# Kernel tuning notes

Hardware: AMD Instinct MI355X
Metric: run time of the kernel (lower is better)

The kernel has to match this reference:

```python
import jax, jax.numpy as jnp
import numpy as np

SEQ, BATCH, HIDDEN = 2048, 2, 2048
NUM_HEADS = 16
HEAD_DIM = HIDDEN // NUM_HEADS  # 128


def setup_inputs() -> dict:
    key = jax.random.key(0)
    k1, k2, k3, k4, k5 = jax.random.split(key, 5)
    scale = 1.0 / np.sqrt(HIDDEN)
    return {
        "hidden_states": jax.random.normal(k1, (SEQ, BATCH, HIDDEN), dtype=jnp.float32),
        "w_qkv": jax.random.normal(k2, (3 * HIDDEN, HIDDEN), dtype=jnp.float32) * scale,
        "b_qkv": jax.random.normal(k3, (3 * HIDDEN,), dtype=jnp.float32) * 0.01,
        "w_dense": jax.random.normal(k4, (HIDDEN, HIDDEN), dtype=jnp.float32) * scale,
        "b_dense": jax.random.normal(k5, (HIDDEN,), dtype=jnp.float32) * 0.01,
    }


def reference(hidden_states, w_qkv, b_qkv, w_dense, b_dense):
    s, b, H = hidden_states.shape
    nh, d = NUM_HEADS, HEAD_DIM
    norm_factor = jnp.asarray(np.sqrt(d), dtype=hidden_states.dtype)

    # QKV projection: [s, b, 3H] -> [s, b, nh, 3d] -> chunk into q, k, v
    mixed = hidden_states @ w_qkv.T + b_qkv
    mixed = mixed.reshape(s, b, nh, 3 * d)
    q, k, v = jnp.split(mixed, 3, axis=-1)  # each [s, b, nh, d]

    # Causal scaled dot-product attention, materializing [b, nh, sq, sk]
    scores = jnp.einsum("sbhd,tbhd->bhst", q, k) / norm_factor
    causal = jnp.tril(jnp.ones((s, s), dtype=bool))  # [sq, sk]
    scores = jnp.where(causal[None, None, :, :], scores, jnp.asarray(-10000.0, scores.dtype))
    probs = jax.nn.softmax(scores, axis=-1)

    # Context: [s, b, nh, d] -> [s, b, H]
    ctx = jnp.einsum("bhst,tbhd->sbhd", probs, v).reshape(s, b, H)

    # Output projection
    return ctx @ w_dense.T + b_dense
```

## Files before the change

### kernel.cpp

```cpp
#include <hip/hip_runtime.h>
#include <stdint.h>
#include <stddef.h>

#define SEQ   2048
#define BATCH 2
#define HID   2048
#define NH    16
#define HD    128
#define MTOT  (SEQ*BATCH)
#define NQKV  (3*HID)
#define KDIM  HID
#define LOG2E 1.4426950408889634f

#define BK64    64
#define NT64    (KDIM/BK64)

typedef short  bf16x8 __attribute__((ext_vector_type(8)));
typedef float  f32x4  __attribute__((ext_vector_type(4)));

__device__ __forceinline__ unsigned short f2bf(float f) {
  union { float f; uint32_t u; } a; a.f = f;
  uint32_t r = a.u + 0x7fffu + ((a.u >> 16) & 1u);
  return (unsigned short)(r >> 16);
}

__device__ __forceinline__ f32x4 mfma16(bf16x8 a, bf16x8 b, f32x4 c) {
  return __builtin_amdgcn_mfma_f32_16x16x32_bf16(a, b, c, 0, 0, 0);
}

__device__ __forceinline__ void gl_lds16(const unsigned short* g, unsigned short* l) {
  __builtin_amdgcn_global_load_lds(
      (const __attribute__((address_space(1))) void*)g,
      (__attribute__((address_space(3))) void*)l, 16, 0, 0);
}

__global__ void cvt3_f32_bf16(const float* __restrict__ a, unsigned short* __restrict__ oa, int na,
                              const float* __restrict__ b, unsigned short* __restrict__ ob, int nb,
                              const float* __restrict__ c, unsigned short* __restrict__ oc, int nc) {
  int i = blockIdx.x * blockDim.x + threadIdx.x;
  int stride = gridDim.x * blockDim.x;
  int ntot = na + nb + nc;
  for (; i < ntot; i += stride) {
    const float* src; unsigned short* dst; int j;
    if (i < na)           { src = a; dst = oa; j = i; }
    else if (i < na + nb) { src = b; dst = ob; j = i - na; }
    else                  { src = c; dst = oc; j = i - na - nb; }
    float4 f = reinterpret_cast<const float4*>(src)[j];
    ushort4 o;
    o.x = f2bf(f.x); o.y = f2bf(f.y); o.z = f2bf(f.z); o.w = f2bf(f.w);
    reinterpret_cast<ushort4*>(dst)[j] = o;
  }
}


#define QBUFS 28672

#define QSTA(R) gl_lds16(Asrc + (size_t)(R) * KDIM + koff, &db[((R) + w * 8) * 64])
#define QSTB(R) gl_lds16(Bsrc + (size_t)(R) * KDIM + koff, &db[16384 + ((R) + w * 8) * 64])

#define RD_A4(R0_,R1_,R2_,R3_, G, SB) do {                                    \
    R0_ = *(const bf16x8*)&(SB)[abase + (2*(G)    ) * 1024 + ga0];            \
    R1_ = *(const bf16x8*)&(SB)[abase + (2*(G)    ) * 1024 + ga1];            \
    R2_ = *(const bf16x8*)&(SB)[abase + (2*(G) + 1) * 1024 + ga0];            \
    R3_ = *(const bf16x8*)&(SB)[abase + (2*(G) + 1) * 1024 + ga1];            \
  } while (0)

#define RD_B6(BQ, SB) do {                                                    \
    BQ[0] = *(const bf16x8*)&(SB)[bbase + 0 * 1024 + ga0];                    \
    BQ[1] = *(const bf16x8*)&(SB)[bbase + 1 * 1024 + ga0];                    \
    BQ[2] = *(const bf16x8*)&(SB)[bbase + 2 * 1024 + ga0];                    \
    BQ[3] = *(const bf16x8*)&(SB)[bbase + 0 * 1024 + ga1];                    \
    BQ[4] = *(const bf16x8*)&(SB)[bbase + 1 * 1024 + ga1];                    \
    BQ[5] = *(const bf16x8*)&(SB)[bbase + 2 * 1024 + ga1];                    \
  } while (0)

#define QPH(G, A0_,A1_,A2_,A3_, RDOP, STOP, VMOP, BQ) do {                    \
    STOP;                                                                     \
    VMOP;                                                                     \
    asm volatile("s_barrier" ::: "memory");                                   \
    RDOP;                                                                     \
    __builtin_amdgcn_sched_barrier(0);                                        \
    __builtin_amdgcn_s_setprio(1);                                            \
    _Pragma("unroll")                                                         \
    for (int n_ = 0; n_ < 3; ++n_) {                                          \
      acc[2*(G)][n_]     = mfma16(A0_, BQ[n_],     acc[2*(G)][n_]);           \
      acc[2*(G)][n_]     = mfma16(A1_, BQ[n_ + 3], acc[2*(G)][n_]);           \
      acc[2*(G) + 1][n_] = mfma16(A2_, BQ[n_],     acc[2*(G) + 1][n_]);       \
      acc[2*(G) + 1][n_] = mfma16(A3_, BQ[n_ + 3], acc[2*(G) + 1][n_]);       \
    }                                                                         \
    __builtin_amdgcn_sched_barrier(0);                                        \
    __builtin_amdgcn_s_setprio(0);                                            \
    asm volatile("s_barrier" ::: "memory");                                   \
  } while (0)

#define VM4  asm volatile("s_waitcnt vmcnt(4)" ::: "memory")
#define VM2  asm volatile("s_waitcnt vmcnt(2)" ::: "memory")
#define VM0  asm volatile("s_waitcnt vmcnt(0)" ::: "memory")

#define QTILE(SB, BQC, ST0, ST1, ST2, ST3, VP1, VP3, RAOP) do {               \
    QPH(0, aX0,aX1,aX2,aX3, RD_A4(aY0,aY1,aY2,aY3, 1, SB), ST0, (void)0, BQC);\
    QPH(1, aY0,aY1,aY2,aY3, RD_A4(aX0,aX1,aX2,aX3, 2, SB), ST1, VP1,     BQC);\
    QPH(2, aX0,aX1,aX2,aX3, RD_A4(aY0,aY1,aY2,aY3, 3, SB), ST2, (void)0, BQC);\
    QPH(3, aY0,aY1,aY2,aY3, RAOP,                          ST3, VP3,     BQC);\
  } while (0)

__global__ __launch_bounds__(512, 2) void qkv_gemm(
    const unsigned short* __restrict__ A,
    const unsigned short* __restrict__ B,
    const float* __restrict__ bias,
    unsigned short* __restrict__ Qo,
    unsigned short* __restrict__ Ko,
    unsigned short* __restrict__ Vt)
{
  __shared__ unsigned short smb[2 * QBUFS];
  const int id  = blockIdx.x;
  const int swz = (id & 7) * 64 + (id >> 3);
  const int m0 = (swz >> 5) * 256, n0 = (swz & 31) * 192;
  const int t = threadIdx.x, l = t & 63, w = t >> 6;
  const int wm = w >> 2, wn = w & 3;
  const int fr = l & 15, fg = l >> 4;
  const int abase = (wm * 128 + fr) * 64;
  const int bbase = 16384 + (wn * 48 + fr) * 64;
  const int ga0 = ((fg     ) ^ (fr & 7)) * 8;
  const int ga1 = ((fg + 4 ) ^ (fr & 7)) * 8;
  const int srcrow = w * 8 + (l >> 3);
  const int sgr    = ((l & 7) ^ (l >> 3)) * 8;
  const unsigned short* Asrc = A + (size_t)(m0 + srcrow) * KDIM + sgr;
  const unsigned short* Bsrc = B + (size_t)(n0 + srcrow) * KDIM + sgr;
  unsigned short* const buf0 = smb;
  unsigned short* const buf1 = smb + QBUFS;

  f32x4 acc[8][3] = {};
  bf16x8 aX0, aX1, aX2, aX3, aY0, aY1, aY2, aY3;
  bf16x8 bqE[6], bqO[6];

  {
    unsigned short* db = buf0;
    size_t koff = 0;
    QSTB(0); QSTB(64); QSTB(128);
    QSTA(0); QSTA(128); QSTA(64); QSTA(192);
  }
  VM2;
  asm volatile("s_barrier" ::: "memory");
  RD_B6(bqE, buf0);
  RD_A4(aX0, aX1, aX2, aX3, 0, buf0);

#pragma unroll 1
  for (int tp = 0; tp < 15; ++tp) {
    {
      unsigned short* db = buf1;
      size_t koff = (size_t)(2 * tp + 1) * BK64;
      QTILE(buf0, bqE,
            QSTB(0); QSTB(64),
            QSTB(128); QSTA(0),
            QSTA(128); QSTA(64),
            QSTA(192),
            VM4, VM2,
            RD_B6(bqO, buf1); RD_A4(aX0,aX1,aX2,aX3, 0, buf1));
    }
    {
      unsigned short* db = buf0;
      size_t koff = (size_t)(2 * tp + 2) * BK64;
      QTILE(buf1, bqO,
            QSTB(0); QSTB(64),
            QSTB(128); QSTA(0),
            QSTA(128); QSTA(64),
            QSTA(192),
            VM4, VM2,
            RD_B6(bqE, buf0); RD_A4(aX0,aX1,aX2,aX3, 0, buf0));
    }
  }
  {
    unsigned short* db = buf1;
    size_t koff = (size_t)31 * BK64;
    QTILE(buf0, bqE,
          QSTB(0); QSTB(64),
          QSTB(128); QSTA(0),
          QSTA(128); QSTA(64),
          QSTA(192),
          VM4, VM2,
          RD_B6(bqO, buf1); RD_A4(aX0,aX1,aX2,aX3, 0, buf1));
  }
  {
    QTILE(buf1, bqO,
          (void)0, (void)0, (void)0, (void)0,
          VM0, (void)0,
          (void)0);
  }

#pragma unroll
  for (int n = 0; n < 3; ++n) {
    int ncol = n0 + wn * 48 + n * 16 + fr;
    float bv = bias[ncol];
    int head = ncol / 384;
    int rem  = ncol - head * 384;
    int wi   = rem >> 7;
    int d    = rem & 127;
#pragma unroll
    for (int m = 0; m < 8; ++m) {
#pragma unroll
      for (int j = 0; j < 4; ++j) {
        int r = m0 + wm * 128 + m * 16 + fg * 4 + j;
        int s = r >> 1, bb = r & 1;
        float val = acc[m][n][j] + bv;
        if (wi == 0) {
          val *= 0.08838834764831845f;
          Qo[(((size_t)(bb * NH + head)) * SEQ + s) * HD + d] = f2bf(val);
        } else if (wi == 1) {
          Ko[(((size_t)(bb * NH + head)) * SEQ + s) * HD + d] = f2bf(val);
        } else {
          Vt[(((size_t)(bb * NH + head)) * HD + d) * SEQ + s] = f2bf(val);
        }
      }
    }
  }
}


#define GEMM_PRE()                                                            \
  const int t = threadIdx.x, l = t & 63, w = t >> 6;                          \
  const int wm = w >> 1, wn = w & 1;                                          \
  const int fr = l & 15, fg = l >> 4;                                         \
  const int fx = fr & 7;                                                      \
  const int srow = l >> 3;                                                    \
  const int sgr  = ((l & 7) ^ srow) * 8;                                      \
  const unsigned short* Aw = A + (size_t)(m0 + w * 32 + srow) * KDIM + sgr;   \
  const unsigned short* Bw = B + (size_t)(n0 + w * 16 + srow) * KDIM + sgr;   \
  unsigned short* smb = &sm[0][0];                                            \
  const int a0 = (wm * 64 + fr) * 64 + ((fg ^ fx) * 8);                       \
  const int a1 = (wm * 64 + fr) * 64 + (((4 + fg) ^ fx) * 8);                 \
  const int b0 = 16384 + (wn * 64 + fr) * 64 + ((fg ^ fx) * 8);               \
  const int b1 = 16384 + (wn * 64 + fr) * 64 + (((4 + fg) ^ fx) * 8);         \
  f32x4 acc[4][4] = {};

#define STAGE_AB(KT) do {                                                     \
    unsigned short* dst = &smb[((KT) % 3) * 24576];                           \
    const unsigned short* ap = Aw + (size_t)(KT) * BK64;                      \
    gl_lds16(ap,                    &dst[(w * 4 + 0) * 512]);                 \
    gl_lds16(ap + 8  * KDIM,        &dst[(w * 4 + 1) * 512]);                 \
    gl_lds16(ap + 16 * KDIM,        &dst[(w * 4 + 2) * 512]);                 \
    gl_lds16(ap + 24 * KDIM,        &dst[(w * 4 + 3) * 512]);                 \
    const unsigned short* bp = Bw + (size_t)(KT) * BK64;                      \
    gl_lds16(bp,                    &dst[16384 + (w * 2 + 0) * 512]);         \
    gl_lds16(bp + 8 * KDIM,         &dst[16384 + (w * 2 + 1) * 512]);         \
  } while (0)

#define GEMM_BODY(KT, VM, DOSTAGE) do {                                       \
    const unsigned short* sb = &smb[((KT) % 3) * 24576];                      \
    if (DOSTAGE) STAGE_AB((KT) + 2);                                          \
    bf16x8 af0[4], af1[4], bg0[4], bg1[4];                                    \
    _Pragma("unroll")                                                         \
    for (int m_ = 0; m_ < 4; ++m_) {                                          \
      af0[m_] = *(const bf16x8*)&sb[a0 + m_ * 1024];                          \
      af1[m_] = *(const bf16x8*)&sb[a1 + m_ * 1024];                          \
    }                                                                         \
    _Pragma("unroll")                                                         \
    for (int n_ = 0; n_ < 4; ++n_) {                                          \
      bg0[n_] = *(const bf16x8*)&sb[b0 + n_ * 1024];                          \
      bg1[n_] = *(const bf16x8*)&sb[b1 + n_ * 1024];                          \
    }                                                                         \
    asm volatile("s_waitcnt vmcnt(" #VM ")" ::: "memory");                    \
    asm volatile("s_barrier" ::: "memory");                                   \
    asm volatile("s_waitcnt lgkmcnt(0)" ::: "memory");                        \
    __builtin_amdgcn_sched_barrier(0);                                        \
    __builtin_amdgcn_s_setprio(1);                                            \
    _Pragma("unroll")                                                         \
    for (int m_ = 0; m_ < 4; ++m_)                                            \
      _Pragma("unroll")                                                       \
      for (int n_ = 0; n_ < 4; ++n_)                                          \
        acc[m_][n_] = mfma16(af0[m_], bg0[n_], acc[m_][n_]);                  \
    _Pragma("unroll")                                                         \
    for (int m_ = 0; m_ < 4; ++m_)                                            \
      _Pragma("unroll")                                                       \
      for (int n_ = 0; n_ < 4; ++n_)                                          \
        acc[m_][n_] = mfma16(af1[m_], bg1[n_], acc[m_][n_]);                  \
    __builtin_amdgcn_sched_barrier(0);                                        \
    __builtin_amdgcn_s_setprio(0);                                            \
    asm volatile("s_barrier" ::: "memory");                                   \
  } while (0)

#define GEMM_MAIN()                                                           \
  STAGE_AB(0); STAGE_AB(1);                                                   \
  asm volatile("s_waitcnt vmcnt(6)" ::: "memory");                            \
  asm volatile("s_barrier" ::: "memory");                                     \
  _Pragma("unroll 1")                                                         \
  for (int kt = 0; kt < NT64 - 2; ++kt)                                       \
    GEMM_BODY(kt, 6, 1);                                                      \
  GEMM_BODY(NT64 - 2, 0, 0);                                                  \
  GEMM_BODY(NT64 - 1, 0, 0);

__global__ __launch_bounds__(512, 1) void dense_gemm(
    const unsigned short* __restrict__ A,
    const unsigned short* __restrict__ B,
    const float* __restrict__ bias,
    float* __restrict__ out)
{
  __shared__ unsigned short sm[3][24576];
  int id  = blockIdx.x;
  int swz = (id & 7) * (gridDim.x >> 3) + (id >> 3);
  const int m0 = (swz / 16) * 256, n0 = (swz % 16) * 128;
  GEMM_PRE();
  GEMM_MAIN();

  const int g4 = fg * 4;
#pragma unroll
  for (int n = 0; n < 4; ++n) {
    int ncol = n0 + wn * 64 + n * 16 + fr;
    float bv = bias[ncol];
#pragma unroll
    for (int m = 0; m < 4; ++m) {
#pragma unroll
      for (int j = 0; j < 4; ++j) {
        int r = m0 + wm * 64 + m * 16 + g4 + j;
        out[(size_t)r * HID + ncol] = acc[m][n][j] + bv;
      }
    }
  }
}

__global__ __launch_bounds__(256, 2) void attn_fwd(
    const unsigned short* __restrict__ Q,
    const unsigned short* __restrict__ K,
    const unsigned short* __restrict__ Vt,
    unsigned short* __restrict__ ctx)
{
  __shared__ unsigned short Ksh[2][64 * 128];
  __shared__ unsigned short Vsh[2][128 * 64];
  __shared__ unsigned short Psh[4][16 * 72];
  const int t = threadIdx.x, l = t & 63, w = t >> 6;
  int nwg = gridDim.x * gridDim.y;
  int id  = blockIdx.y * gridDim.x + blockIdx.x;
  int swz = (id & 7) * (nwg >> 3) + (id >> 3);
  const int pair = swz & 15;
  const int bh   = swz >> 4;
  const int qtA = pair, qtB = 31 - pair;
  const int fr = l & 15, fg = l >> 4;
  const size_t base  = (size_t)bh * SEQ * HD;
  const size_t vbase = (size_t)bh * HD * SEQ;

#define STAGE(BUF, KT) do {                                                   \
    const unsigned short* Kt_ = K + base + (size_t)((KT) * 64) * HD;          \
    _Pragma("unroll")                                                         \
    for (int i_ = 0; i_ < 4; ++i_) {                                          \
      int ch_  = w * 4 + i_;                                                  \
      int row_ = ch_ * 4 + (l >> 4);                                          \
      int c16_ = (l & 15) ^ (row_ & 7);                                       \
      gl_lds16(Kt_ + (size_t)row_ * HD + c16_ * 8, &Ksh[BUF][ch_ * 512]);     \
    }                                                                         \
    const unsigned short* Vg_ = Vt + vbase + (KT) * 64;                       \
    _Pragma("unroll")                                                         \
    for (int i_ = 0; i_ < 4; ++i_) {                                          \
      int ch_  = w * 4 + i_;                                                  \
      int row_ = ch_ * 8 + (l >> 3);                                          \
      int c16_ = (l & 7) ^ (row_ & 7);                                        \
      gl_lds16(Vg_ + (size_t)row_ * SEQ + c16_ * 8, &Vsh[BUF][ch_ * 512]);    \
    }                                                                         \
  } while (0)

#define COMPUTE_TILE(QF, OACC, MROW, LROW, QT) do {                           \
    f32x4 sacc[4] = {};                                                       \
    _Pragma("unroll")                                                         \
    for (int c_ = 0; c_ < 4; ++c_) {                                          \
      _Pragma("unroll")                                                       \
      for (int n_ = 0; n_ < 4; ++n_) {                                        \
        int krow = n_ * 16 + fr;                                              \
        int g_   = (c_ * 4 + fg) ^ (krow & 7);                                \
        bf16x8 kf = *(const bf16x8*)&Ksh[buf][krow * 128 + g_ * 8];           \
        sacc[n_] = mfma16(QF[c_], kf, sacc[n_]);                              \
      }                                                                       \
    }                                                                         \
    if (kt == (QT)) {                                                         \
      _Pragma("unroll")                                                       \
      for (int n_ = 0; n_ < 4; ++n_)                                          \
        _Pragma("unroll")                                                     \
        for (int j_ = 0; j_ < 4; ++j_)                                        \
          if (n_ * 16 + fr > w * 16 + fg * 4 + j_) sacc[n_][j_] = -1e30f;     \
    }                                                                         \
    float tm_[4];                                                             \
    _Pragma("unroll")                                                         \
    for (int j_ = 0; j_ < 4; ++j_) {                                          \
      float v0 = fmaxf(fmaxf(sacc[0][j_], sacc[1][j_]),                       \
                       fmaxf(sacc[2][j_], sacc[3][j_]));                      \
      v0 = fmaxf(v0, __shfl_xor(v0, 1));                                      \
      v0 = fmaxf(v0, __shfl_xor(v0, 2));                                      \
      v0 = fmaxf(v0, __shfl_xor(v0, 4));                                      \
      v0 = fmaxf(v0, __shfl_xor(v0, 8));                                      \
      tm_[j_] = v0;                                                           \
    }                                                                         \
    float sc_[4], ps_[4];                                                     \
    _Pragma("unroll")                                                         \
    for (int j_ = 0; j_ < 4; ++j_) {                                          \
      float mn_ = fmaxf(MROW[j_], tm_[j_]);                                   \
      sc_[j_] = exp2f((MROW[j_] - mn_) * LOG2E);                              \
      MROW[j_] = mn_;                                                         \
      ps_[j_] = 0.f;                                                          \
    }                                                                         \
    _Pragma("unroll")                                                         \
    for (int n_ = 0; n_ < 4; ++n_)                                            \
      _Pragma("unroll")                                                       \
      for (int j_ = 0; j_ < 4; ++j_) {                                        \
        float p_ = exp2f((sacc[n_][j_] - MROW[j_]) * LOG2E);                  \
        sacc[n_][j_] = p_;                                                    \
        ps_[j_] += p_;                                                        \
      }                                                                       \
    _Pragma("unroll")                                                         \
    for (int j_ = 0; j_ < 4; ++j_) {                                          \
      float s_ = ps_[j_];                                                     \
      s_ += __shfl_xor(s_, 1);                                                \
      s_ += __shfl_xor(s_, 2);                                                \
      s_ += __shfl_xor(s_, 4);                                                \
      s_ += __shfl_xor(s_, 8);                                                \
      LROW[j_] = LROW[j_] * sc_[j_] + s_;                                     \
    }                                                                         \
    _Pragma("unroll")                                                         \
    for (int n_ = 0; n_ < 8; ++n_)                                            \
      _Pragma("unroll")                                                       \
      for (int j_ = 0; j_ < 4; ++j_)                                          \
        OACC[n_][j_] *= sc_[j_];                                              \
    _Pragma("unroll")                                                         \
    for (int n_ = 0; n_ < 4; ++n_)                                            \
      _Pragma("unroll")                                                       \
      for (int j_ = 0; j_ < 4; ++j_)                                          \
        Psh[w][(fg * 4 + j_) * 72 + n_ * 16 + fr] = f2bf(sacc[n_][j_]);       \
    _Pragma("unroll")                                                         \
    for (int ks_ = 0; ks_ < 2; ++ks_) {                                       \
      bf16x8 pf = *(const bf16x8*)&Psh[w][fr * 72 + ks_ * 32 + fg * 8];       \
      _Pragma("unroll")                                                       \
      for (int n_ = 0; n_ < 8; ++n_) {                                        \
        int vrow = n_ * 16 + fr;                                              \
        int g_   = (ks_ * 4 + fg) ^ (vrow & 7);                               \
        bf16x8 vf = *(const bf16x8*)&Vsh[buf][vrow * 64 + g_ * 8];            \
        OACC[n_] = mfma16(pf, vf, OACC[n_]);                                  \
      }                                                                       \
    }                                                                         \
  } while (0)

  bf16x8 qfA[4], qfB[4];
  {
    const unsigned short* qpA = Q + base + (size_t)(qtA * 64 + w * 16 + fr) * HD + fg * 8;
    const unsigned short* qpB = Q + base + (size_t)(qtB * 64 + w * 16 + fr) * HD + fg * 8;
#pragma unroll
    for (int c = 0; c < 4; ++c) {
      qfA[c] = *(const bf16x8*)(qpA + c * 32);
      qfB[c] = *(const bf16x8*)(qpB + c * 32);
    }
  }
  f32x4 oaccA[8] = {}, oaccB[8] = {};
  float mA[4] = {-1e30f, -1e30f, -1e30f, -1e30f};
  float mB[4] = {-1e30f, -1e30f, -1e30f, -1e30f};
  float lA[4] = {0.f, 0.f, 0.f, 0.f};
  float lB[4] = {0.f, 0.f, 0.f, 0.f};

  STAGE(0, 0);
  __syncthreads();
  int buf = 0;
  for (int kt = 0; kt <= qtB; ++kt) {
    if (kt < qtB) STAGE(buf ^ 1, kt + 1);
    COMPUTE_TILE(qfB, oaccB, mB, lB, qtB);
    if (kt <= qtA) COMPUTE_TILE(qfA, oaccA, mA, lA, qtA);
    __syncthreads();
    buf ^= 1;
  }

  const int bb = bh >> 4, h = bh & 15;
#define WRITE_CTX(OACC, LROW, QT) do {                                        \
    _Pragma("unroll")                                                         \
    for (int n_ = 0; n_ < 8; ++n_)                                            \
      _Pragma("unroll")                                                       \
      for (int j_ = 0; j_ < 4; ++j_) {                                        \
        int qrow = (QT) * 64 + w * 16 + fg * 4 + j_;                          \
        float val = OACC[n_][j_] / LROW[j_];                                  \
        ctx[((size_t)(qrow * BATCH + bb)) * HID + h * HD + n_ * 16 + fr] =    \
            f2bf(val);                                                        \
      }                                                                       \
  } while (0)
  WRITE_CTX(oaccA, lA, qtA);
  WRITE_CTX(oaccB, lB, qtB);
#undef STAGE
#undef COMPUTE_TILE
#undef WRITE_CTX
}

extern "C" void kernel_launch(void* const* d_in, const int* in_sizes, int n_in,
                              void* d_out, int out_size, void* d_ws, size_t ws_size,
                              hipStream_t stream) {
  const float* hs      = (const float*)d_in[0];
  const float* w_qkv   = (const float*)d_in[1];
  const float* b_qkv   = (const float*)d_in[2];
  const float* w_dense = (const float*)d_in[3];
  const float* b_dense = (const float*)d_in[4];
  float* out = (float*)d_out;

  unsigned short* hsb = (unsigned short*)d_ws;
  unsigned short* wqb = hsb + (size_t)MTOT * HID;
  unsigned short* wdb = wqb + (size_t)NQKV * HID;
  unsigned short* q   = wdb + (size_t)HID * HID;
  unsigned short* k   = q   + (size_t)MTOT * HID;
  unsigned short* vt  = k   + (size_t)MTOT * HID;
  unsigned short* ctx = vt  + (size_t)MTOT * HID;

  cvt3_f32_bf16<<<2048, 256, 0, stream>>>(
      hs, hsb, (MTOT * HID) / 4,
      w_qkv, wqb, (NQKV * HID) / 4,
      w_dense, wdb, (HID * HID) / 4);

  qkv_gemm<<<dim3((MTOT / 256) * (NQKV / 192)), 512, 0, stream>>>(hsb, wqb, b_qkv, q, k, vt);
  attn_fwd<<<dim3(16, 32), 256, 0, stream>>>(q, k, vt, ctx);
  dense_gemm<<<dim3((MTOT / 256) * (HID / 128)), 512, 0, stream>>>(ctx, wdb, b_dense, out);
}
```

Baseline: 279.9 us.

## Simplify QKV and dense GEMM pipelines to single-barrier double-buffered tiles

Both GEMM main loops are restructured. The QKV GEMM drops its four-phase, eight-barrier ping-pong schedule for a simple double-buffered loop with one barrier and full vmcnt/lgkmcnt drains per K-tile. The dense GEMM goes from a three-stage LDS ring to two buffers, staging the next tile while interleaving A-fragment reads with MFMAs. This cuts barrier and sched_barrier overhead and shrinks LDS use for the dense kernel. In exchange it gives up deeper prefetch and priority tuning, so global-load latency may be exposed once per tile.

Measured after the change: 276.6 us. Within noise of the previous version (-1.2%).

```diff
diff --git a/kernel.cpp b/kernel.cpp
--- a/kernel.cpp
+++ b/kernel.cpp
@@ -57,15 +57,17 @@
 
 #define QSTA(R) gl_lds16(Asrc + (size_t)(R) * KDIM + koff, &db[((R) + w * 8) * 64])
 #define QSTB(R) gl_lds16(Bsrc + (size_t)(R) * KDIM + koff, &db[16384 + ((R) + w * 8) * 64])
-
-#define RD_A4(R0_,R1_,R2_,R3_, G, SB) do {                                    \
-    R0_ = *(const bf16x8*)&(SB)[abase + (2*(G)    ) * 1024 + ga0];            \
-    R1_ = *(const bf16x8*)&(SB)[abase + (2*(G)    ) * 1024 + ga1];            \
-    R2_ = *(const bf16x8*)&(SB)[abase + (2*(G) + 1) * 1024 + ga0];            \
-    R3_ = *(const bf16x8*)&(SB)[abase + (2*(G) + 1) * 1024 + ga1];            \
-  } while (0)
-
-#define RD_B6(BQ, SB) do {                                                    \
+#define QSTAGE7 do { QSTB(0); QSTB(64); QSTB(128);                            \
+                     QSTA(0); QSTA(64); QSTA(128); QSTA(192); } while (0)
+
+#define RD_A4v(R, G, SB) do {                                                 \
+    R[0] = *(const bf16x8*)&(SB)[abase + (2*(G)    ) * 1024 + ga0];           \
+    R[1] = *(const bf16x8*)&(SB)[abase + (2*(G)    ) * 1024 + ga1];           \
+    R[2] = *(const bf16x8*)&(SB)[abase + (2*(G) + 1) * 1024 + ga0];           \
+    R[3] = *(const bf16x8*)&(SB)[abase + (2*(G) + 1) * 1024 + ga1];           \
+  } while (0)
+
+#define RD_B6v(BQ, SB) do {                                                   \
     BQ[0] = *(const bf16x8*)&(SB)[bbase + 0 * 1024 + ga0];                    \
     BQ[1] = *(const bf16x8*)&(SB)[bbase + 1 * 1024 + ga0];                    \
     BQ[2] = *(const bf16x8*)&(SB)[bbase + 2 * 1024 + ga0];                    \
@@ -74,34 +76,31 @@
     BQ[5] = *(const bf16x8*)&(SB)[bbase + 2 * 1024 + ga1];                    \
   } while (0)
 
-#define QPH(G, A0_,A1_,A2_,A3_, RDOP, STOP, VMOP, BQ) do {                    \
-    STOP;                                                                     \
-    VMOP;                                                                     \
+#define MFMA_G(G, R, BQ) do {                                                 \
+    _Pragma("unroll")                                                         \
+    for (int n_ = 0; n_ < 3; ++n_) {                                          \
+      acc[2*(G)][n_]     = mfma16(R[0], BQ[n_],     acc[2*(G)][n_]);          \
+      acc[2*(G)][n_]     = mfma16(R[1], BQ[n_ + 3], acc[2*(G)][n_]);          \
+      acc[2*(G) + 1][n_] = mfma16(R[2], BQ[n_],     acc[2*(G) + 1][n_]);      \
+      acc[2*(G) + 1][n_] = mfma16(R[3], BQ[n_ + 3], acc[2*(G) + 1][n_]);      \
+    }                                                                         \
+  } while (0)
+
+#define QTILE_FF(SB, DOSTAGE) do {                                            \
+    bf16x8 bq[6], aP[4], aQ[4];                                               \
+    RD_B6v(bq, SB);                                                           \
+    RD_A4v(aP, 0, SB);                                                        \
+    RD_A4v(aQ, 1, SB);                                                        \
+    if (DOSTAGE) QSTAGE7;                                                     \
+    MFMA_G(0, aP, bq);                                                        \
+    RD_A4v(aP, 2, SB);                                                        \
+    MFMA_G(1, aQ, bq);                                                        \
+    RD_A4v(aQ, 3, SB);                                                        \
+    MFMA_G(2, aP, bq);                                                        \
+    MFMA_G(3, aQ, bq);                                                        \
+    asm volatile("s_waitcnt lgkmcnt(0)" ::: "memory");                        \
+    asm volatile("s_waitcnt vmcnt(0)" ::: "memory");                          \
     asm volatile("s_barrier" ::: "memory");                                   \
-    RDOP;                                                                     \
-    __builtin_amdgcn_sched_barrier(0);                                        \
-    __builtin_amdgcn_s_setprio(1);                                            \
-    _Pragma("unroll")                                                         \
-    for (int n_ = 0; n_ < 3; ++n_) {                                          \
-      acc[2*(G)][n_]     = mfma16(A0_, BQ[n_],     acc[2*(G)][n_]);           \
-      acc[2*(G)][n_]     = mfma16(A1_, BQ[n_ + 3], acc[2*(G)][n_]);           \
-      acc[2*(G) + 1][n_] = mfma16(A2_, BQ[n_],     acc[2*(G) + 1][n_]);       \
-      acc[2*(G) + 1][n_] = mfma16(A3_, BQ[n_ + 3], acc[2*(G) + 1][n_]);       \
-    }                                                                         \
-    __builtin_amdgcn_sched_barrier(0);                                        \
-    __builtin_amdgcn_s_setprio(0);                                            \
-    asm volatile("s_barrier" ::: "memory");                                   \
-  } while (0)
-
-#define VM4  asm volatile("s_waitcnt vmcnt(4)" ::: "memory")
-#define VM2  asm volatile("s_waitcnt vmcnt(2)" ::: "memory")
-#define VM0  asm volatile("s_waitcnt vmcnt(0)" ::: "memory")
-
-#define QTILE(SB, BQC, ST0, ST1, ST2, ST3, VP1, VP3, RAOP) do {               \
-    QPH(0, aX0,aX1,aX2,aX3, RD_A4(aY0,aY1,aY2,aY3, 1, SB), ST0, (void)0, BQC);\
-    QPH(1, aY0,aY1,aY2,aY3, RD_A4(aX0,aX1,aX2,aX3, 2, SB), ST1, VP1,     BQC);\
-    QPH(2, aX0,aX1,aX2,aX3, RD_A4(aY0,aY1,aY2,aY3, 3, SB), ST2, (void)0, BQC);\
-    QPH(3, aY0,aY1,aY2,aY3, RAOP,                          ST3, VP3,     BQC);\
   } while (0)
 
 __global__ __launch_bounds__(512, 2) void qkv_gemm(
@@ -127,65 +126,23 @@
   const int sgr    = ((l & 7) ^ (l >> 3)) * 8;
   const unsigned short* Asrc = A + (size_t)(m0 + srcrow) * KDIM + sgr;
   const unsigned short* Bsrc = B + (size_t)(n0 + srcrow) * KDIM + sgr;
-  unsigned short* const buf0 = smb;
-  unsigned short* const buf1 = smb + QBUFS;
 
   f32x4 acc[8][3] = {};
-  bf16x8 aX0, aX1, aX2, aX3, aY0, aY1, aY2, aY3;
-  bf16x8 bqE[6], bqO[6];
 
   {
-    unsigned short* db = buf0;
+    unsigned short* db = smb;
     size_t koff = 0;
-    QSTB(0); QSTB(64); QSTB(128);
-    QSTA(0); QSTA(128); QSTA(64); QSTA(192);
-  }
-  VM2;
+    QSTAGE7;
+  }
+  asm volatile("s_waitcnt vmcnt(0)" ::: "memory");
   asm volatile("s_barrier" ::: "memory");
-  RD_B6(bqE, buf0);
-  RD_A4(aX0, aX1, aX2, aX3, 0, buf0);
 
 #pragma unroll 1
-  for (int tp = 0; tp < 15; ++tp) {
-    {
-      unsigned short* db = buf1;
-      size_t koff = (size_t)(2 * tp + 1) * BK64;
-      QTILE(buf0, bqE,
-            QSTB(0); QSTB(64),
-            QSTB(128); QSTA(0),
-            QSTA(128); QSTA(64),
-            QSTA(192),
-            VM4, VM2,
-            RD_B6(bqO, buf1); RD_A4(aX0,aX1,aX2,aX3, 0, buf1));
-    }
-    {
-      unsigned short* db = buf0;
-      size_t koff = (size_t)(2 * tp + 2) * BK64;
-      QTILE(buf1, bqO,
-            QSTB(0); QSTB(64),
-            QSTB(128); QSTA(0),
-            QSTA(128); QSTA(64),
-            QSTA(192),
-            VM4, VM2,
-            RD_B6(bqE, buf0); RD_A4(aX0,aX1,aX2,aX3, 0, buf0));
-    }
-  }
-  {
-    unsigned short* db = buf1;
-    size_t koff = (size_t)31 * BK64;
-    QTILE(buf0, bqE,
-          QSTB(0); QSTB(64),
-          QSTB(128); QSTA(0),
-          QSTA(128); QSTA(64),
-          QSTA(192),
-          VM4, VM2,
-          RD_B6(bqO, buf1); RD_A4(aX0,aX1,aX2,aX3, 0, buf1));
-  }
-  {
-    QTILE(buf1, bqO,
-          (void)0, (void)0, (void)0, (void)0,
-          VM0, (void)0,
-          (void)0);
+  for (int kt = 0; kt < NT64; ++kt) {
+    const unsigned short* sb = &smb[(kt & 1) * QBUFS];
+    unsigned short* db = &smb[((kt + 1) & 1) * QBUFS];
+    size_t koff = (size_t)(kt + 1) * BK64;
+    QTILE_FF(sb, (kt < NT64 - 1));
   }
 
 #pragma unroll
@@ -217,77 +174,49 @@
 }
 
 
-#define GEMM_PRE()                                                            \
-  const int t = threadIdx.x, l = t & 63, w = t >> 6;                          \
-  const int wm = w >> 1, wn = w & 1;                                          \
-  const int fr = l & 15, fg = l >> 4;                                         \
-  const int fx = fr & 7;                                                      \
-  const int srow = l >> 3;                                                    \
-  const int sgr  = ((l & 7) ^ srow) * 8;                                      \
-  const unsigned short* Aw = A + (size_t)(m0 + w * 32 + srow) * KDIM + sgr;   \
-  const unsigned short* Bw = B + (size_t)(n0 + w * 16 + srow) * KDIM + sgr;   \
-  unsigned short* smb = &sm[0][0];                                            \
-  const int a0 = (wm * 64 + fr) * 64 + ((fg ^ fx) * 8);                       \
-  const int a1 = (wm * 64 + fr) * 64 + (((4 + fg) ^ fx) * 8);                 \
-  const int b0 = 16384 + (wn * 64 + fr) * 64 + ((fg ^ fx) * 8);               \
-  const int b1 = 16384 + (wn * 64 + fr) * 64 + (((4 + fg) ^ fx) * 8);         \
-  f32x4 acc[4][4] = {};
-
-#define STAGE_AB(KT) do {                                                     \
-    unsigned short* dst = &smb[((KT) % 3) * 24576];                           \
-    const unsigned short* ap = Aw + (size_t)(KT) * BK64;                      \
-    gl_lds16(ap,                    &dst[(w * 4 + 0) * 512]);                 \
-    gl_lds16(ap + 8  * KDIM,        &dst[(w * 4 + 1) * 512]);                 \
-    gl_lds16(ap + 16 * KDIM,        &dst[(w * 4 + 2) * 512]);                 \
-    gl_lds16(ap + 24 * KDIM,        &dst[(w * 4 + 3) * 512]);                 \
-    const unsigned short* bp = Bw + (size_t)(KT) * BK64;                      \
-    gl_lds16(bp,                    &dst[16384 + (w * 2 + 0) * 512]);         \
-    gl_lds16(bp + 8 * KDIM,         &dst[16384 + (w * 2 + 1) * 512]);         \
-  } while (0)
-
-#define GEMM_BODY(KT, VM, DOSTAGE) do {                                       \
-    const unsigned short* sb = &smb[((KT) % 3) * 24576];                      \
-    if (DOSTAGE) STAGE_AB((KT) + 2);                                          \
-    bf16x8 af0[4], af1[4], bg0[4], bg1[4];                                    \
-    _Pragma("unroll")                                                         \
-    for (int m_ = 0; m_ < 4; ++m_) {                                          \
-      af0[m_] = *(const bf16x8*)&sb[a0 + m_ * 1024];                          \
-      af1[m_] = *(const bf16x8*)&sb[a1 + m_ * 1024];                          \
-    }                                                                         \
+#define DBUFS 24576
+
+#define DSTAGE6 do {                                                          \
+    gl_lds16(Aw + koff,                    &db[(w * 4 + 0) * 512]);           \
+    gl_lds16(Aw + koff + 8  * KDIM,        &db[(w * 4 + 1) * 512]);           \
+    gl_lds16(Aw + koff + 16 * KDIM,        &db[(w * 4 + 2) * 512]);           \
+    gl_lds16(Aw + koff + 24 * KDIM,        &db[(w * 4 + 3) * 512]);           \
+    gl_lds16(Bw + koff,                    &db[16384 + (w * 2 + 0) * 512]);   \
+    gl_lds16(Bw + koff + 8 * KDIM,         &db[16384 + (w * 2 + 1) * 512]);   \
+  } while (0)
+
+#define MFMA_D(X, Y, M) do {                                                  \
     _Pragma("unroll")                                                         \
     for (int n_ = 0; n_ < 4; ++n_) {                                          \
-      bg0[n_] = *(const bf16x8*)&sb[b0 + n_ * 1024];                          \
-      bg1[n_] = *(const bf16x8*)&sb[b1 + n_ * 1024];                          \
-    }                                                                         \
-    asm volatile("s_waitcnt vmcnt(" #VM ")" ::: "memory");                    \
+      acc[M][n_] = mfma16(X, bg0[n_], acc[M][n_]);                            \
+      acc[M][n_] = mfma16(Y, bg1[n_], acc[M][n_]);                            \
+    }                                                                         \
+  } while (0)
+
+#define DTILE_FF(SB, DOSTAGE) do {                                            \
+    bf16x8 bg0[4], bg1[4], e0, e1, o0, o1;                                    \
+    _Pragma("unroll")                                                         \
+    for (int n_ = 0; n_ < 4; ++n_) {                                          \
+      bg0[n_] = *(const bf16x8*)&(SB)[b0 + n_ * 1024];                        \
+      bg1[n_] = *(const bf16x8*)&(SB)[b1 + n_ * 1024];                        \
+    }                                                                         \
+    e0 = *(const bf16x8*)&(SB)[a0];                                           \
+    e1 = *(const bf16x8*)&(SB)[a1];                                           \
+    o0 = *(const bf16x8*)&(SB)[a0 + 1024];                                    \
+    o1 = *(const bf16x8*)&(SB)[a1 + 1024];                                    \
+    if (DOSTAGE) DSTAGE6;                                                     \
+    MFMA_D(e0, e1, 0);                                                        \
+    e0 = *(const bf16x8*)&(SB)[a0 + 2048];                                    \
+    e1 = *(const bf16x8*)&(SB)[a1 + 2048];                                    \
+    MFMA_D(o0, o1, 1);                                                        \
+    o0 = *(const bf16x8*)&(SB)[a0 + 3072];                                    \
+    o1 = *(const bf16x8*)&(SB)[a1 + 3072];                                    \
+    MFMA_D(e0, e1, 2);                                                        \
+    MFMA_D(o0, o1, 3);                                                        \
+    asm volatile("s_waitcnt lgkmcnt(0)" ::: "memory");                        \
+    asm volatile("s_waitcnt vmcnt(0)" ::: "memory");                          \
     asm volatile("s_barrier" ::: "memory");                                   \
-    asm volatile("s_waitcnt lgkmcnt(0)" ::: "memory");                        \
-    __builtin_amdgcn_sched_barrier(0);                                        \
-    __builtin_amdgcn_s_setprio(1);                                            \
-    _Pragma("unroll")                                                         \
-    for (int m_ = 0; m_ < 4; ++m_)                                            \
-      _Pragma("unroll")                                                       \
-      for (int n_ = 0; n_ < 4; ++n_)                                          \
-        acc[m_][n_] = mfma16(af0[m_], bg0[n_], acc[m_][n_]);                  \
-    _Pragma("unroll")                                                         \
-    for (int m_ = 0; m_ < 4; ++m_)                                            \
-      _Pragma("unroll")                                                       \
-      for (int n_ = 0; n_ < 4; ++n_)                                          \
-        acc[m_][n_] = mfma16(af1[m_], bg1[n_], acc[m_][n_]);                  \
-    __builtin_amdgcn_sched_barrier(0);                                        \
-    __builtin_amdgcn_s_setprio(0);                                            \
-    asm volatile("s_barrier" ::: "memory");                                   \
-  } while (0)
-
-#define GEMM_MAIN()                                                           \
-  STAGE_AB(0); STAGE_AB(1);                                                   \
-  asm volatile("s_waitcnt vmcnt(6)" ::: "memory");                            \
-  asm volatile("s_barrier" ::: "memory");                                     \
-  _Pragma("unroll 1")                                                         \
-  for (int kt = 0; kt < NT64 - 2; ++kt)                                       \
-    GEMM_BODY(kt, 6, 1);                                                      \
-  GEMM_BODY(NT64 - 2, 0, 0);                                                  \
-  GEMM_BODY(NT64 - 1, 0, 0);
+  } while (0)
 
 __global__ __launch_bounds__(512, 1) void dense_gemm(
     const unsigned short* __restrict__ A,
@@ -295,12 +224,39 @@
     const float* __restrict__ bias,
     float* __restrict__ out)
 {
-  __shared__ unsigned short sm[3][24576];
+  __shared__ unsigned short smd[2 * DBUFS];
   int id  = blockIdx.x;
   int swz = (id & 7) * (gridDim.x >> 3) + (id >> 3);
   const int m0 = (swz / 16) * 256, n0 = (swz % 16) * 128;
-  GEMM_PRE();
-  GEMM_MAIN();
+  const int t = threadIdx.x, l = t & 63, w = t >> 6;
+  const int wm = w >> 1, wn = w & 1;
+  const int fr = l & 15, fg = l >> 4;
+  const int fx = fr & 7;
+  const int srow = l >> 3;
+  const int sgr  = ((l & 7) ^ srow) * 8;
+  const unsigned short* Aw = A + (size_t)(m0 + w * 32 + srow) * KDIM + sgr;
+  const unsigned short* Bw = B + (size_t)(n0 + w * 16 + srow) * KDIM + sgr;
+  const int a0 = (wm * 64 + fr) * 64 + ((fg ^ fx) * 8);
+  const int a1 = (wm * 64 + fr) * 64 + (((4 + fg) ^ fx) * 8);
+  const int b0 = 16384 + (wn * 64 + fr) * 64 + ((fg ^ fx) * 8);
+  const int b1 = 16384 + (wn * 64 + fr) * 64 + (((4 + fg) ^ fx) * 8);
+  f32x4 acc[4][4] = {};
+
+  {
+    unsigned short* db = smd;
+    size_t koff = 0;
+    DSTAGE6;
+  }
+  asm volatile("s_waitcnt vmcnt(0)" ::: "memory");
+  asm volatile("s_barrier" ::: "memory");
+
+#pragma unroll 1
+  for (int kt = 0; kt < NT64; ++kt) {
+    const unsigned short* sb = &smd[(kt & 1) * DBUFS];
+    unsigned short* db = &smd[((kt + 1) & 1) * DBUFS];
+    size_t koff = (size_t)(kt + 1) * BK64;
+    DTILE_FF(sb, (kt < NT64 - 1));
+  }
 
   const int g4 = fg * 4;
 #pragma unroll
```
